# Performance work log

Hardware: AMD Instinct MI355X
Metric: run time of the kernel (lower is better)

The kernel has to match this reference:

```python
import jax, jax.numpy as jnp
from jax import lax
import numpy as np

B, T, H, P = 256, 2048, 256, 24

def setup_inputs() -> dict:
    key = jax.random.key(0)
    ks = jax.random.split(key, 7)
    s_ih = 1.0 / np.sqrt(H)
    return {
        "x": jax.random.normal(ks[0], (B, T, 1), dtype=jnp.float32),
        "W_ih": jax.random.normal(ks[1], (H, 1), dtype=jnp.float32) * s_ih,
        "W_hh": jax.random.normal(ks[2], (H, H), dtype=jnp.float32) * s_ih,
        "b_ih": jax.random.normal(ks[3], (H,), dtype=jnp.float32) * s_ih,
        "b_hh": jax.random.normal(ks[4], (H,), dtype=jnp.float32) * s_ih,
        "W_out": jax.random.normal(ks[5], (P, H), dtype=jnp.float32) * s_ih,
        "b_out": jax.random.normal(ks[6], (P,), dtype=jnp.float32) * s_ih,
    }

def reference(x, W_ih, W_hh, b_ih, b_hh, W_out, b_out):
    # Precompute input projection for all timesteps: [B,T,H]
    xp = jnp.einsum('bti,hi->bth', x, W_ih) + b_ih + b_hh
    h0 = jnp.zeros((x.shape[0], W_hh.shape[0]), dtype=x.dtype)

    def step(h, xt):  # xt: [B,H]
        h_new = jnp.tanh(xt + h @ W_hh.T)
        return h_new, None

    hT, _ = lax.scan(step, h0, xp.transpose(1, 0, 2))  # scan over T
    # Linear head on last hidden state: [B,P]
    return hT @ W_out.T + b_out
```

## Files before the change

kernel.cpp:

```cpp
#include <hip/hip_runtime.h>


#define BB 256
#define TT 2048
#define HH 256
#define PP 24

typedef _Float16 half_t;
typedef _Float16 h8v __attribute__((ext_vector_type(8)));
typedef float    f4v __attribute__((ext_vector_type(4)));

__device__ __forceinline__ f4v mfma16(h8v a, h8v b, f4v c) {
    return __builtin_amdgcn_mfma_f32_16x16x32_f16(a, b, c, 0, 0, 0);
}

__device__ __forceinline__ void lds_barrier() {
    asm volatile("s_waitcnt lgkmcnt(0)\n\ts_barrier" ::: "memory");
}

__global__ __launch_bounds__(512, 2)
void rnn_persist(const float* __restrict__ x,
                 const float* __restrict__ W_ih,
                 const float* __restrict__ W_hh,
                 const float* __restrict__ b_ih,
                 const float* __restrict__ b_hh,
                 const float* __restrict__ W_out,
                 const float* __restrict__ b_out,
                 float* __restrict__ out)
{
    __shared__ __align__(16) half_t hbuf[2][HH];

    const int tid  = threadIdx.x;
    const int b    = blockIdx.x;
    const int w    = tid >> 6;
    const int l    = tid & 63;
    const int ln   = l & 15;
    const int kg   = l >> 4;

    hbuf[0][tid & 255] = (half_t)0.f;

    h8v wf[2][8];
    #pragma unroll
    for (int rb = 0; rb < 2; ++rb) {
        #pragma unroll
        for (int kb = 0; kb < 8; ++kb) {
            const float* p = W_hh + (size_t)(32 * w + 16 * rb + ln) * HH
                                   + 32 * kb + 8 * kg;
            const float4 qa = *(const float4*)p;
            const float4 qb = *(const float4*)(p + 4);
            wf[rb][kb] = (h8v){(half_t)qa.x, (half_t)qa.y, (half_t)qa.z,
                               (half_t)qa.w, (half_t)qb.x, (half_t)qb.y,
                               (half_t)qb.z, (half_t)qb.w};
        }
    }

    float wihv[2], cbv[2];
    #pragma unroll
    for (int rb = 0; rb < 2; ++rb) {
        const int o = 32 * w + 16 * rb + ln;
        wihv[rb] = W_ih[o];
        cbv[rb]  = b_ih[o] + b_hh[o];
    }
    const bool writer = (l < 16);

    __syncthreads();

    const float* xb = x + b * TT;
    const f4v zf = {0.f, 0.f, 0.f, 0.f};

    auto step = [&](const half_t* __restrict__ cur, half_t* __restrict__ nxt,
                    float xt) __attribute__((always_inline)) {
        const h8v* hp = (const h8v*)(cur + 8 * kg);
        h8v af[8];
        #pragma unroll
        for (int kb = 0; kb < 8; ++kb) af[kb] = hp[4 * kb];

        const float u0p = fmaf(xt, wihv[0], cbv[0]);
        const float u1p = fmaf(xt, wihv[1], cbv[1]);

        __builtin_amdgcn_s_setprio(1);
        f4v a00 = mfma16(af[0], wf[0][0], zf);
        f4v a01 = mfma16(af[4], wf[0][4], zf);
        a00 = mfma16(af[1], wf[0][1], a00);
        a01 = mfma16(af[5], wf[0][5], a01);
        a00 = mfma16(af[2], wf[0][2], a00);
        a01 = mfma16(af[6], wf[0][6], a01);
        a00 = mfma16(af[3], wf[0][3], a00);
        a01 = mfma16(af[7], wf[0][7], a01);
        f4v a10 = mfma16(af[0], wf[1][0], zf);
        f4v a11 = mfma16(af[4], wf[1][4], zf);
        a10 = mfma16(af[1], wf[1][1], a10);
        a11 = mfma16(af[5], wf[1][5], a11);
        a10 = mfma16(af[2], wf[1][2], a10);
        a11 = mfma16(af[6], wf[1][6], a11);
        a10 = mfma16(af[3], wf[1][3], a10);
        a11 = mfma16(af[7], wf[1][7], a11);
        __builtin_amdgcn_s_setprio(0);

        if (writer) {
            const float y0 = a00.x + a01.x;
            const float u0 = u0p + y0;
            const float p0 = __builtin_amdgcn_exp2f(u0 * 2.8853900817779268f);
            const float t0 = fmaf(-2.f, __builtin_amdgcn_rcpf(p0 + 1.f), 1.f);
            nxt[32 * w + ln] = (half_t)t0;
            const float y1 = a10.x + a11.x;
            const float u1 = u1p + y1;
            const float p1 = __builtin_amdgcn_exp2f(u1 * 2.8853900817779268f);
            const float t1 = fmaf(-2.f, __builtin_amdgcn_rcpf(p1 + 1.f), 1.f);
            nxt[32 * w + 16 + ln] = (half_t)t1;
        }
        lds_barrier();
    };

    float4 xa = *(const float4*)(xb + 0);
    float4 xc = *(const float4*)(xb + 4);
    for (int t = 0; t < TT; t += 8) {
        const int tn = (t + 8 < TT) ? (t + 8) : t;
        const float4 xa_n = *(const float4*)(xb + tn);
        const float4 xc_n = *(const float4*)(xb + tn + 4);
        step(hbuf[0], hbuf[1], xa.x);
        step(hbuf[1], hbuf[0], xa.y);
        step(hbuf[0], hbuf[1], xa.z);
        step(hbuf[1], hbuf[0], xa.w);
        step(hbuf[0], hbuf[1], xc.x);
        step(hbuf[1], hbuf[0], xc.y);
        step(hbuf[0], hbuf[1], xc.z);
        step(hbuf[1], hbuf[0], xc.w);
        xa = xa_n;
        xc = xc_n;
    }

    if (tid < PP) {
        const float* wo = W_out + tid * HH;
        float s0 = 0.f, s1 = 0.f, s2 = 0.f, s3 = 0.f;
        #pragma unroll
        for (int h = 0; h < HH; h += 4) {
            s0 = fmaf(wo[h + 0], (float)hbuf[0][h + 0], s0);
            s1 = fmaf(wo[h + 1], (float)hbuf[0][h + 1], s1);
            s2 = fmaf(wo[h + 2], (float)hbuf[0][h + 2], s2);
            s3 = fmaf(wo[h + 3], (float)hbuf[0][h + 3], s3);
        }
        out[b * PP + tid] = b_out[tid] + (s0 + s1) + (s2 + s3);
    }
}

extern "C" void kernel_launch(void* const* d_in, const int* in_sizes, int n_in,
                              void* d_out, int out_size, void* d_ws, size_t ws_size,
                              hipStream_t stream) {
    const float* x     = (const float*)d_in[0];
    const float* W_ih  = (const float*)d_in[1];
    const float* W_hh  = (const float*)d_in[2];
    const float* b_ih  = (const float*)d_in[3];
    const float* b_hh  = (const float*)d_in[4];
    const float* W_out = (const float*)d_in[5];
    const float* b_out = (const float*)d_in[6];
    float* out = (float*)d_out;

    rnn_persist<<<BB, 512, 0, stream>>>(x, W_ih, W_hh, b_ih, b_hh, W_out, b_out, out);
}
```

Measured before the change: 844.2 us.

## Split hidden rows between MFMA waves and packed-dot VALU waves with DPP reduction

Waves 0-3 keep the MFMA path for hidden rows 0-127. Waves 4-7 now compute rows 128-255 with fdot2 packed-half dot products on the VALU, reducing across lanes with DPP adds. The hidden-state LDS buffer is padded to a stride of 24 halves per 16 elements, and every index is remapped through hidx16. The goal is to run the matrix and vector units at the same time within each serial timestep, and to cut LDS bank conflicts. The cost is more register pressure, since each VALU thread holds 64 h2 weights, plus a more complex reduction, and the DPP lane pattern could be wrong.

After: 1.054 ms. +24.8%, slower.

```diff
diff --git a/kernel.cpp b/kernel.cpp
--- a/kernel.cpp
+++ b/kernel.cpp
@@ -5,17 +5,42 @@
 #define TT 2048
 #define HH 256
 #define PP 24
+#define HSTRH 24
 
 typedef _Float16 half_t;
+typedef _Float16 h2  __attribute__((ext_vector_type(2)));
 typedef _Float16 h8v __attribute__((ext_vector_type(8)));
 typedef float    f4v __attribute__((ext_vector_type(4)));
 
+struct alignas(16) hoct { h2 v[4]; };
+
+__device__ __forceinline__ int hidx16(int k) { return (k >> 4) * HSTRH + (k & 15); }
+
+template<int CTRL>
+__device__ __forceinline__ float dppadd(float dst, float src) {
+    return dst + __int_as_float(__builtin_amdgcn_update_dpp(
+        0, __float_as_int(src), CTRL, 0xf, 0xf, true));
+}
+
+__device__ __forceinline__ float fdot2f(h2 a, h2 b, float c) {
+#if __has_builtin(__builtin_amdgcn_fdot2)
+    return __builtin_amdgcn_fdot2(a, b, c, false);
+#else
+    return fmaf((float)a.x, (float)b.x, fmaf((float)a.y, (float)b.y, c));
+#endif
+}
+
 __device__ __forceinline__ f4v mfma16(h8v a, h8v b, f4v c) {
     return __builtin_amdgcn_mfma_f32_16x16x32_f16(a, b, c, 0, 0, 0);
 }
 
 __device__ __forceinline__ void lds_barrier() {
     asm volatile("s_waitcnt lgkmcnt(0)\n\ts_barrier" ::: "memory");
+}
+
+__device__ __forceinline__ float tanh_fast(float u) {
+    const float p = __builtin_amdgcn_exp2f(u * 2.8853900817779268f);
+    return fmaf(-2.f, __builtin_amdgcn_rcpf(p + 1.f), 1.f);
 }
 
 __global__ __launch_bounds__(512, 2)
@@ -28,38 +53,63 @@
                  const float* __restrict__ b_out,
                  float* __restrict__ out)
 {
-    __shared__ __align__(16) half_t hbuf[2][HH];
-
-    const int tid  = threadIdx.x;
-    const int b    = blockIdx.x;
-    const int w    = tid >> 6;
-    const int l    = tid & 63;
-    const int ln   = l & 15;
-    const int kg   = l >> 4;
-
-    hbuf[0][tid & 255] = (half_t)0.f;
+    __shared__ __align__(16) half_t hbuf[2][16 * HSTRH];
+
+    const int tid = threadIdx.x;
+    const int b   = blockIdx.x;
+    const int w   = tid >> 6;
+    const int l   = tid & 63;
+    const bool is_mfma = (w < 4);
+
+    hbuf[0][hidx16(tid & 255)] = (half_t)0.f;
+
+    const int ln = l & 15;
+    const int kg = l >> 4;
+    const int aoff = 24 * (kg >> 1) + 8 * (kg & 1);
 
     h8v wf[2][8];
-    #pragma unroll
-    for (int rb = 0; rb < 2; ++rb) {
-        #pragma unroll
-        for (int kb = 0; kb < 8; ++kb) {
-            const float* p = W_hh + (size_t)(32 * w + 16 * rb + ln) * HH
-                                   + 32 * kb + 8 * kg;
-            const float4 qa = *(const float4*)p;
-            const float4 qb = *(const float4*)(p + 4);
-            wf[rb][kb] = (h8v){(half_t)qa.x, (half_t)qa.y, (half_t)qa.z,
-                               (half_t)qa.w, (half_t)qb.x, (half_t)qb.y,
-                               (half_t)qb.z, (half_t)qb.w};
-        }
-    }
-
     float wihv[2], cbv[2];
-    #pragma unroll
-    for (int rb = 0; rb < 2; ++rb) {
-        const int o = 32 * w + 16 * rb + ln;
-        wihv[rb] = W_ih[o];
-        cbv[rb]  = b_ih[o] + b_hh[o];
+    const int tid2 = tid & 255;
+    const int c    = tid2 & 15;
+    const int g2   = tid2 >> 4;
+    h2 w2h[8][8];
+    float wihS = 0.f, cbS = 0.f;
+    int  widxS = 0;
+
+    if (is_mfma) {
+        #pragma unroll
+        for (int rb = 0; rb < 2; ++rb) {
+            #pragma unroll
+            for (int kb = 0; kb < 8; ++kb) {
+                const float* p = W_hh + (size_t)(32 * w + 16 * rb + ln) * HH
+                                       + 32 * kb + 8 * kg;
+                const float4 qa = *(const float4*)p;
+                const float4 qb = *(const float4*)(p + 4);
+                wf[rb][kb] = (h8v){(half_t)qa.x, (half_t)qa.y, (half_t)qa.z,
+                                   (half_t)qa.w, (half_t)qb.x, (half_t)qb.y,
+                                   (half_t)qb.z, (half_t)qb.w};
+            }
+        }
+        #pragma unroll
+        for (int rb = 0; rb < 2; ++rb) {
+            const int o = 32 * w + 16 * rb + ln;
+            wihv[rb] = W_ih[o];
+            cbv[rb]  = b_ih[o] + b_hh[o];
+        }
+    } else {
+        const int m[8] = {0, 2, 7, 5, 8, 10, 15, 13};
+        #pragma unroll
+        for (int s = 0; s < 8; ++s) {
+            const int row_idx = 128 + 8 * g2 + ((c ^ m[s]) >> 1);
+            const float* row = W_hh + (size_t)row_idx * HH + 16 * c;
+            #pragma unroll
+            for (int j = 0; j < 8; ++j)
+                w2h[s][j] = (h2){(half_t)row[2 * j], (half_t)row[2 * j + 1]};
+        }
+        const int o = 128 + 8 * g2 + (c >> 1);
+        wihS  = W_ih[o];
+        cbS   = b_ih[o] + b_hh[o];
+        widxS = hidx16(o);
     }
     const bool writer = (l < 16);
 
@@ -70,44 +120,74 @@
 
     auto step = [&](const half_t* __restrict__ cur, half_t* __restrict__ nxt,
                     float xt) __attribute__((always_inline)) {
-        const h8v* hp = (const h8v*)(cur + 8 * kg);
-        h8v af[8];
-        #pragma unroll
-        for (int kb = 0; kb < 8; ++kb) af[kb] = hp[4 * kb];
-
-        const float u0p = fmaf(xt, wihv[0], cbv[0]);
-        const float u1p = fmaf(xt, wihv[1], cbv[1]);
-
-        __builtin_amdgcn_s_setprio(1);
-        f4v a00 = mfma16(af[0], wf[0][0], zf);
-        f4v a01 = mfma16(af[4], wf[0][4], zf);
-        a00 = mfma16(af[1], wf[0][1], a00);
-        a01 = mfma16(af[5], wf[0][5], a01);
-        a00 = mfma16(af[2], wf[0][2], a00);
-        a01 = mfma16(af[6], wf[0][6], a01);
-        a00 = mfma16(af[3], wf[0][3], a00);
-        a01 = mfma16(af[7], wf[0][7], a01);
-        f4v a10 = mfma16(af[0], wf[1][0], zf);
-        f4v a11 = mfma16(af[4], wf[1][4], zf);
-        a10 = mfma16(af[1], wf[1][1], a10);
-        a11 = mfma16(af[5], wf[1][5], a11);
-        a10 = mfma16(af[2], wf[1][2], a10);
-        a11 = mfma16(af[6], wf[1][6], a11);
-        a10 = mfma16(af[3], wf[1][3], a10);
-        a11 = mfma16(af[7], wf[1][7], a11);
-        __builtin_amdgcn_s_setprio(0);
-
-        if (writer) {
-            const float y0 = a00.x + a01.x;
-            const float u0 = u0p + y0;
-            const float p0 = __builtin_amdgcn_exp2f(u0 * 2.8853900817779268f);
-            const float t0 = fmaf(-2.f, __builtin_amdgcn_rcpf(p0 + 1.f), 1.f);
-            nxt[32 * w + ln] = (half_t)t0;
-            const float y1 = a10.x + a11.x;
-            const float u1 = u1p + y1;
-            const float p1 = __builtin_amdgcn_exp2f(u1 * 2.8853900817779268f);
-            const float t1 = fmaf(-2.f, __builtin_amdgcn_rcpf(p1 + 1.f), 1.f);
-            nxt[32 * w + 16 + ln] = (half_t)t1;
+        if (is_mfma) {
+            const half_t* ap = cur + aoff;
+            h8v af[8];
+            #pragma unroll
+            for (int kb = 0; kb < 8; ++kb)
+                af[kb] = *(const h8v*)(ap + 48 * kb);
+
+            const float u0p = fmaf(xt, wihv[0], cbv[0]);
+            const float u1p = fmaf(xt, wihv[1], cbv[1]);
+
+            __builtin_amdgcn_s_setprio(1);
+            f4v a00 = mfma16(af[0], wf[0][0], zf);
+            f4v a01 = mfma16(af[4], wf[0][4], zf);
+            a00 = mfma16(af[1], wf[0][1], a00);
+            a01 = mfma16(af[5], wf[0][5], a01);
+            a00 = mfma16(af[2], wf[0][2], a00);
+            a01 = mfma16(af[6], wf[0][6], a01);
+            a00 = mfma16(af[3], wf[0][3], a00);
+            a01 = mfma16(af[7], wf[0][7], a01);
+            f4v a10 = mfma16(af[0], wf[1][0], zf);
+            f4v a11 = mfma16(af[4], wf[1][4], zf);
+            a10 = mfma16(af[1], wf[1][1], a10);
+            a11 = mfma16(af[5], wf[1][5], a11);
+            a10 = mfma16(af[2], wf[1][2], a10);
+            a11 = mfma16(af[6], wf[1][6], a11);
+            a10 = mfma16(af[3], wf[1][3], a10);
+            a11 = mfma16(af[7], wf[1][7], a11);
+            __builtin_amdgcn_s_setprio(0);
+
+            if (writer) {
+                const float t0 = tanh_fast(u0p + (a00.x + a01.x));
+                nxt[hidx16(32 * w + ln)] = (half_t)t0;
+                const float t1 = tanh_fast(u1p + (a10.x + a11.x));
+                nxt[hidx16(32 * w + 16 + ln)] = (half_t)t1;
+            }
+        } else {
+            const hoct* hq = (const hoct*)(cur + c * HSTRH);
+            const hoct qa = hq[0], qb = hq[1];
+
+            float acc[8];
+            #pragma unroll
+            for (int s = 0; s < 8; ++s) acc[s] = fdot2f(w2h[s][0], qa.v[0], 0.f);
+            #pragma unroll
+            for (int s = 0; s < 8; ++s) acc[s] = fdot2f(w2h[s][1], qa.v[1], acc[s]);
+            #pragma unroll
+            for (int s = 0; s < 8; ++s) acc[s] = fdot2f(w2h[s][2], qa.v[2], acc[s]);
+            #pragma unroll
+            for (int s = 0; s < 8; ++s) acc[s] = fdot2f(w2h[s][3], qa.v[3], acc[s]);
+            #pragma unroll
+            for (int s = 0; s < 8; ++s) acc[s] = fdot2f(w2h[s][4], qb.v[0], acc[s]);
+            #pragma unroll
+            for (int s = 0; s < 8; ++s) acc[s] = fdot2f(w2h[s][5], qb.v[1], acc[s]);
+            #pragma unroll
+            for (int s = 0; s < 8; ++s) acc[s] = fdot2f(w2h[s][6], qb.v[2], acc[s]);
+            #pragma unroll
+            for (int s = 0; s < 8; ++s) acc[s] = fdot2f(w2h[s][7], qb.v[3], acc[s]);
+
+            float b0 = dppadd<0x128>(acc[0], acc[4]);
+            float b1 = dppadd<0x128>(acc[1], acc[5]);
+            float b2 = dppadd<0x128>(acc[2], acc[6]);
+            float b3 = dppadd<0x128>(acc[3], acc[7]);
+            float c0 = dppadd<0x141>(b0, b2);
+            float c1 = dppadd<0x141>(b1, b3);
+            float d  = dppadd<0x4E>(c0, c1);
+            float e  = dppadd<0xB1>(d, d);
+
+            const float th = tanh_fast(fmaf(xt, wihS, cbS) + e);
+            nxt[widxS] = (half_t)th;
         }
         lds_barrier();
     };
@@ -135,10 +215,10 @@
         float s0 = 0.f, s1 = 0.f, s2 = 0.f, s3 = 0.f;
         #pragma unroll
         for (int h = 0; h < HH; h += 4) {
-            s0 = fmaf(wo[h + 0], (float)hbuf[0][h + 0], s0);
-            s1 = fmaf(wo[h + 1], (float)hbuf[0][h + 1], s1);
-            s2 = fmaf(wo[h + 2], (float)hbuf[0][h + 2], s2);
-            s3 = fmaf(wo[h + 3], (float)hbuf[0][h + 3], s3);
+            s0 = fmaf(wo[h + 0], (float)hbuf[0][hidx16(h + 0)], s0);
+            s1 = fmaf(wo[h + 1], (float)hbuf[0][hidx16(h + 1)], s1);
+            s2 = fmaf(wo[h + 2], (float)hbuf[0][hidx16(h + 2)], s2);
+            s3 = fmaf(wo[h + 3], (float)hbuf[0][hidx16(h + 3)], s3);
         }
         out[b * PP + tid] = b_out[tid] + (s0 + s1) + (s2 + s3);
     }
```
